# Kernel optimization log

Hardware: AMD Instinct MI355X
Metric: run time of the kernel (lower is better)

The kernel has to match this reference:

```python
import jax, jax.numpy as jnp
import numpy as np
from math import factorial, sqrt

BATCH = 4096
RS_IN = [(16, 0), (16, 1), (16, 2)]   # (mul, l), parity 0
RS_OUT = [(16, 0), (16, 1), (16, 2)]

# selection rule: l_filter in [|l_in-l_out|, l_in+l_out]
SET_LF = sorted({l for (_, li) in RS_IN for (_, lo) in RS_OUT
                 for l in range(abs(li - lo), li + lo + 1)})
Y_OFF = {l: sum(2 * k + 1 for k in SET_LF if k < l) for l in SET_LF}
Y_DIM = sum(2 * l + 1 for l in SET_LF)  # 25


def wigner_3j(j1, j2, j3, m1, m2, m3):
    if m1 + m2 + m3 != 0 or not (abs(j1 - j2) <= j3 <= j1 + j2):
        return 0.0
    if abs(m1) > j1 or abs(m2) > j2 or abs(m3) > j3:
        return 0.0
    f = factorial
    pre = sqrt(f(j1 + j2 - j3) * f(j1 - j2 + j3) * f(-j1 + j2 + j3) / f(j1 + j2 + j3 + 1))
    pre *= sqrt(f(j1 + m1) * f(j1 - m1) * f(j2 + m2) * f(j2 - m2) * f(j3 + m3) * f(j3 - m3))
    s = 0.0
    for t in range(max(0, j2 - j3 - m1, j1 - j3 + m2),
                   min(j1 + j2 - j3, j1 - m1, j2 + m2) + 1):
        s += (-1) ** t / (f(t) * f(j3 - j2 + m1 + t) * f(j3 - j1 - m2 + t)
                          * f(j1 + j2 - j3 - t) * f(j1 - m1 - t) * f(j2 + m2 - t))
    return (-1) ** (j1 - j2 - m3) * pre * s


def real_to_complex(l):
    # A[M+l, m+l]: complex Y^M expressed in the real SH basis
    A = np.zeros((2 * l + 1, 2 * l + 1), dtype=np.complex128)
    A[l, l] = 1.0
    s2 = 1.0 / np.sqrt(2.0)
    for m in range(1, l + 1):
        A[l + m, l + m] = (-1) ** m * s2
        A[l + m, l - m] = 1j * (-1) ** m * s2
        A[l - m, l + m] = s2
        A[l - m, l - m] = -1j * s2
    return A


def clebsch_gordan(l1, l2, l3):
    # real, unit-Frobenius-norm invariant 3-tensor (unique up to sign)
    T = np.zeros((2 * l1 + 1, 2 * l2 + 1, 2 * l3 + 1))
    for m1 in range(-l1, l1 + 1):
        for m2 in range(-l2, l2 + 1):
            m3 = -(m1 + m2)
            if abs(m3) <= l3:
                T[m1 + l1, m2 + l2, m3 + l3] = wigner_3j(l1, l2, l3, m1, m2, m3)
    A1, A2, A3 = real_to_complex(l1), real_to_complex(l2), real_to_complex(l3)
    C = np.einsum('abc,ai,bj,ck->ijk', T, A1.conj(), A2.conj(), A3.conj())
    C = C.real if np.linalg.norm(C.real) >= np.linalg.norm(C.imag) else C.imag
    n = np.linalg.norm(C)
    return (C / n).astype(np.float32) if n > 0 else C.astype(np.float32)


# precompute per-block padded CG tensors and R offsets
R_OFF = {}
C_BLOCKS = {}
_off = 0
for _i, (_mo, _lo) in enumerate(RS_OUT):
    for _j, (_mi, _li) in enumerate(RS_IN):
        _lfs = list(range(abs(_li - _lo), _li + _lo + 1))
        R_OFF[(_i, _j)] = (_off, len(_lfs))
        _off += _mo * _mi * len(_lfs)
        _C = np.zeros((len(_lfs), 2 * _lo + 1, 2 * _li + 1, Y_DIM), dtype=np.float32)
        for _k, _lf in enumerate(_lfs):
            _o = Y_OFF[_lf]
            _C[_k, :, :, _o:_o + 2 * _lf + 1] = clebsch_gordan(_lo, _li, _lf)
        C_BLOCKS[(_i, _j)] = jnp.asarray(_C)
N_PATH = _off  # 4864


def setup_inputs() -> dict:
    key = jax.random.key(0)
    k1, k2, k3 = jax.random.split(key, 3)
    Y = jax.random.normal(k1, (Y_DIM, BATCH), dtype=jnp.float32)
    R = jax.random.normal(k2, (BATCH, N_PATH), dtype=jnp.float32)
    norm_coef = jax.random.uniform(k3, (len(RS_OUT), len(RS_IN), BATCH),
                                   dtype=jnp.float32, minval=0.5, maxval=1.5)
    return {"Y": Y, "R": R, "norm_coef": norm_coef}


def reference(Y, R, norm_coef):
    # Y: [Y_DIM, batch], R: [batch, N_PATH], norm_coef: [3, 3, batch]
    batch = Y.shape[1]
    rows = []
    for i, (mo, lo) in enumerate(RS_OUT):
        row = []
        for j, (mi, li) in enumerate(RS_IN):
            off, nlf = R_OFF[(i, j)]
            sub_R = R[:, off:off + mo * mi * nlf].reshape(batch, mo, mi, nlf)
            # fuse the per-l_filter loop into one contraction over k and m
            K = jnp.einsum('kijm,mz,zuvk,z->zuivj',
                           C_BLOCKS[(i, j)], Y, sub_R, norm_coef[i, j])
            row.append(K.reshape(batch, mo * (2 * lo + 1), mi * (2 * li + 1)))
        rows.append(jnp.concatenate(row, axis=2))
    return jnp.concatenate(rows, axis=1)  # [batch, 144, 144]
```

## Files before the change

kernel.cpp:

```cpp
#include <hip/hip_runtime.h>

#define NPATH 4864
#define YDIM  25
#define NW    259
#define NCG   1225
#define NWP   400


struct Tables {
    float cg[NCG];
    int   woff[NW];
    int   wlf[NW];
    int   wij[NW];
    int   wdst[NW];
};

constexpr double cfact(int n) { double f = 1.0; for (int i = 2; i <= n; ++i) f *= (double)i; return f; }

constexpr double csqrt_(double x) {
    if (x <= 0.0) return 0.0;
    double g = x > 1.0 ? x : 1.0, p = 0.0;
    for (int it = 0; it < 200; ++it) { p = g; g = 0.5 * (g + x / g); if (g == p) break; }
    return g;
}
constexpr int cabs_(int x) { return x < 0 ? -x : x; }
constexpr int cmax3(int a, int b, int c) { int m = a > b ? a : b; return m > c ? m : c; }
constexpr int cmin3(int a, int b, int c) { int m = a < b ? a : b; return m < c ? m : c; }

constexpr double cwig3j(int j1, int j2, int j3, int m1, int m2, int m3) {
    if (m1 + m2 + m3 != 0) return 0.0;
    if (cabs_(m1) > j1 || cabs_(m2) > j2 || cabs_(m3) > j3) return 0.0;
    if (j3 < cabs_(j1 - j2) || j3 > j1 + j2) return 0.0;
    double prod = cfact(j1 + j2 - j3) * cfact(j1 - j2 + j3) * cfact(-j1 + j2 + j3)
                / cfact(j1 + j2 + j3 + 1);
    prod *= cfact(j1 + m1) * cfact(j1 - m1) * cfact(j2 + m2) * cfact(j2 - m2)
          * cfact(j3 + m3) * cfact(j3 - m3);
    double pre = csqrt_(prod);
    int t0 = cmax3(0, j2 - j3 - m1, j1 - j3 + m2);
    int t1 = cmin3(j1 + j2 - j3, j1 - m1, j2 + m2);
    double s = 0.0;
    for (int t = t0; t <= t1; ++t) {
        double d = cfact(t) * cfact(j3 - j2 + m1 + t) * cfact(j3 - j1 - m2 + t)
                 * cfact(j1 + j2 - j3 - t) * cfact(j1 - m1 - t) * cfact(j2 + m2 - t);
        s += ((t & 1) ? -1.0 : 1.0) / d;
    }
    int p = j1 - j2 - m3; p = ((p % 2) + 2) % 2;
    return (p ? -1.0 : 1.0) * pre * s;
}

struct Ent { int col; double re; double im; };

constexpr int arow(int l, int a, Ent* e) {
    int m = a - l;
    double s2 = csqrt_(0.5);
    if (m == 0) { e[0] = Ent{l, 1.0, 0.0}; return 1; }
    if (m > 0) {
        double sgn = (m & 1) ? -1.0 : 1.0;
        e[0] = Ent{l + m, sgn * s2, 0.0};
        e[1] = Ent{l - m, 0.0, sgn * s2};
        return 2;
    }
    int mm = -m;
    e[0] = Ent{l + mm, s2, 0.0};
    e[1] = Ent{l - mm, 0.0, -s2};
    return 2;
}

constexpr Tables make_tables() {
    Tables T{};
    const int CL1[19]  = {0,0,0,1,1,1,1,1,1,1,2,2,2,2,2,2,2,2,2};
    const int CL2[19]  = {0,1,2,0,1,1,1,2,2,2,0,1,1,1,2,2,2,2,2};
    const int CL3[19]  = {0,1,2,1,0,1,2,1,2,3,2,1,2,3,0,1,2,3,4};
    const int COFF[19] = {0,1,10,35,44,53,80,125,170,245,350,375,420,495,600,625,700,825,1000};

    for (int c = 0; c < 19; ++c) {
        int l1 = CL1[c], l2 = CL2[c], l3 = CL3[c], coff = COFF[c];
        int n1 = 2 * l1 + 1, n2 = 2 * l2 + 1, n3 = 2 * l3 + 1, ntot = n1 * n2 * n3;
        double Cre[225] = {}, Cim[225] = {};
        for (int a = 0; a < n1; ++a)
            for (int b = 0; b < n2; ++b) {
                int m1 = a - l1, m2 = b - l2, m3 = -(m1 + m2);
                if (cabs_(m3) > l3) continue;
                double tv = cwig3j(l1, l2, l3, m1, m2, m3);
                if (tv == 0.0) continue;
                int crow = m3 + l3;
                Ent e1[2] = {}, e2[2] = {}, e3[2] = {};
                int k1 = arow(l1, a, e1), k2 = arow(l2, b, e2), k3 = arow(l3, crow, e3);
                for (int x = 0; x < k1; ++x)
                    for (int y = 0; y < k2; ++y)
                        for (int w = 0; w < k3; ++w) {
                            double r1 = e1[x].re, i1 = -e1[x].im;
                            double r2 = e2[y].re, i2 = -e2[y].im;
                            double r3 = e3[w].re, i3 = -e3[w].im;
                            double pr = r1 * r2 - i1 * i2, pi = r1 * i2 + i1 * r2;
                            double qr = pr * r3 - pi * i3, qi = pr * i3 + pi * r3;
                            int idx = (e1[x].col * n2 + e2[y].col) * n3 + e3[w].col;
                            Cre[idx] += tv * qr;
                            Cim[idx] += tv * qi;
                        }
            }
        double sR = 0.0, sI = 0.0;
        for (int i = 0; i < ntot; ++i) { sR += Cre[i] * Cre[i]; sI += Cim[i] * Cim[i]; }
        bool useRe = (sR >= sI);
        double nn = csqrt_(useRe ? sR : sI);
        double inv = nn > 0.0 ? 1.0 / nn : 0.0;
        for (int i = 0; i < ntot; ++i)
            T.cg[coff + i] = (float)((useRe ? Cre[i] : Cim[i]) * inv);
    }

    const int NLFt[9]   = {1,1,1,1,3,3,1,3,5};
    const int CGOFF9[9] = {0,1,10,35,44,125,350,375,600};
    const int WPB[9]  = {0, 4, 8, 16, 20, 56, 128, 136, 200};
    const int PADt[9] = {1, 4, 8,  1,  4,  8,   1,   4,   8};
    int w = 0;
    for (int ij = 0; ij < 9; ++ij) {
        int lo = ij / 3, li = ij % 3;
        int lfmin = lo > li ? lo - li : li - lo;
        int no2 = 2 * lo + 1, ni2 = 2 * li + 1, cgo = CGOFF9[ij];
        for (int k = 0; k < NLFt[ij]; ++k) {
            int lf = lfmin + k;
            for (int a = 0; a < no2; ++a)
                for (int b = 0; b < ni2; ++b) {
                    T.woff[w] = cgo + (a * ni2 + b) * (2 * lf + 1);
                    T.wlf[w]  = lf;
                    T.wij[w]  = ij;
                    T.wdst[w] = WPB[ij] + (k * no2 + a) * PADt[ij] + b;
                    ++w;
                }
            cgo += no2 * ni2 * (2 * lf + 1);
        }
    }
    return T;
}

constexpr Tables H_TAB = make_tables();
__device__ __constant__ Tables d_tab = H_TAB;

template <int I, int J, int NLF, int WPB, int PAD, int ROFF, int ROWB, int COLB>
__device__ __forceinline__ void region(const float* __restrict__ Wp,
                                       const float* __restrict__ Rl,
                                       float* __restrict__ Oz, int u, int v) {
    constexpr int NO2 = 2 * I + 1, NI2 = 2 * J + 1;
    const float* rb = Rl + ROFF + (u * 16 + v) * NLF;
    float Rk[NLF];
#pragma unroll
    for (int k = 0; k < NLF; ++k) Rk[k] = rb[k];

    float acc[NO2][NI2];
#pragma unroll
    for (int a = 0; a < NO2; ++a)
#pragma unroll
        for (int b = 0; b < NI2; ++b) acc[a][b] = 0.f;

#pragma unroll
    for (int k = 0; k < NLF; ++k)
#pragma unroll
        for (int a = 0; a < NO2; ++a) {
            const float* wrow = Wp + WPB + (k * NO2 + a) * PAD;
            if constexpr (NI2 == 1) {
                acc[a][0] += wrow[0] * Rk[k];
            } else if constexpr (NI2 == 3) {
                float4 w4 = *(const float4*)wrow;
                acc[a][0] += w4.x * Rk[k];
                acc[a][1] += w4.y * Rk[k];
                acc[a][2] += w4.z * Rk[k];
            } else {
                float4 w4 = *(const float4*)wrow;
                float  w5 = wrow[4];
                acc[a][0] += w4.x * Rk[k];
                acc[a][1] += w4.y * Rk[k];
                acc[a][2] += w4.z * Rk[k];
                acc[a][3] += w4.w * Rk[k];
                acc[a][4] += w5   * Rk[k];
            }
        }

    float* ob = Oz + (ROWB + u * NO2) * 144 + COLB + v * NI2;
#pragma unroll
    for (int a = 0; a < NO2; ++a)
#pragma unroll
        for (int b = 0; b < NI2; ++b) ob[a * 144 + b] = acc[a][b];
}


__global__ __launch_bounds__(256) void tp_kernel(const float* __restrict__ Yg,
                                                 const float* __restrict__ Rg,
                                                 const float* __restrict__ Ng,
                                                 float* __restrict__ Og, int batch) {
    __shared__ __align__(16) float Rl[NPATH];
    __shared__ __align__(16) float Wp[NWP];
    __shared__ float Ys[YDIM];
    __shared__ float Ns[9];

    int z = blockIdx.x;
    int t = threadIdx.x;

    const float4* Rg4 = (const float4*)(Rg + (size_t)z * NPATH);
    float4* Rl4 = (float4*)Rl;
    for (int p = t; p < NPATH / 4; p += 256) Rl4[p] = Rg4[p];
    if (t < YDIM) Ys[t] = Yg[t * batch + z];
    if (t >= 32 && t < 41) Ns[t - 32] = Ng[(t - 32) * batch + z];
    __syncthreads();

    for (int w = t; w < NW; w += 256) {
        int off = d_tab.woff[w], lf = d_tab.wlf[w];
        float acc = 0.f;
        for (int ci = 0; ci <= 2 * lf; ++ci) acc += d_tab.cg[off + ci] * Ys[lf * lf + ci];
        Wp[d_tab.wdst[w]] = acc * Ns[d_tab.wij[w]];
    }
    __syncthreads();

    float* Oz = Og + (size_t)z * 20736;
    int u = t >> 4, v = t & 15;

    region<0, 0, 1,   0, 1,     0,  0,  0>(Wp, Rl, Oz, u, v);
    region<0, 1, 1,   4, 4,   256,  0, 16>(Wp, Rl, Oz, u, v);
    region<0, 2, 1,   8, 8,   512,  0, 64>(Wp, Rl, Oz, u, v);
    region<1, 0, 1,  16, 1,   768, 16,  0>(Wp, Rl, Oz, u, v);
    region<1, 1, 3,  20, 4,  1024, 16, 16>(Wp, Rl, Oz, u, v);
    region<1, 2, 3,  56, 8,  1792, 16, 64>(Wp, Rl, Oz, u, v);
    region<2, 0, 1, 128, 1,  2560, 64,  0>(Wp, Rl, Oz, u, v);
    region<2, 1, 3, 136, 4,  2816, 64, 16>(Wp, Rl, Oz, u, v);
    region<2, 2, 5, 200, 8,  3584, 64, 64>(Wp, Rl, Oz, u, v);
}

extern "C" void kernel_launch(void* const* d_in, const int* in_sizes, int n_in,
                              void* d_out, int out_size, void* d_ws, size_t ws_size,
                              hipStream_t stream) {
    const float* Y = (const float*)d_in[0];
    const float* R = (const float*)d_in[1];
    const float* N = (const float*)d_in[2];
    float* O = (float*)d_out;
    int batch = in_sizes[0] / YDIM;

    hipLaunchKernelGGL(tp_kernel, dim3(batch), dim3(256), 0, stream, Y, R, N, O, batch);
}
```

Measured before the change: 417.1 us.

## Split each batch element across two 128-thread blocks and read R directly from global

```diff
diff --git a/kernel.cpp b/kernel.cpp
--- a/kernel.cpp
+++ b/kernel.cpp
@@ -138,10 +138,10 @@
 
 template <int I, int J, int NLF, int WPB, int PAD, int ROFF, int ROWB, int COLB>
 __device__ __forceinline__ void region(const float* __restrict__ Wp,
-                                       const float* __restrict__ Rl,
+                                       const float* __restrict__ Rz,
                                        float* __restrict__ Oz, int u, int v) {
     constexpr int NO2 = 2 * I + 1, NI2 = 2 * J + 1;
-    const float* rb = Rl + ROFF + (u * 16 + v) * NLF;
+    const float* rb = Rz + ROFF + (u * 16 + v) * NLF;
     float Rk[NLF];
 #pragma unroll
     for (int k = 0; k < NLF; ++k) Rk[k] = rb[k];
@@ -183,45 +183,39 @@
 }
 
 
-__global__ __launch_bounds__(256) void tp_kernel(const float* __restrict__ Yg,
+__global__ __launch_bounds__(128) void tp_kernel(const float* __restrict__ Yg,
                                                  const float* __restrict__ Rg,
                                                  const float* __restrict__ Ng,
                                                  float* __restrict__ Og, int batch) {
-    __shared__ __align__(16) float Rl[NPATH];
     __shared__ __align__(16) float Wp[NWP];
-    __shared__ float Ys[YDIM];
-    __shared__ float Ns[9];
-
-    int z = blockIdx.x;
+
+    int bid = blockIdx.x;
+    int z = bid >> 1, h = bid & 1;
     int t = threadIdx.x;
 
-    const float4* Rg4 = (const float4*)(Rg + (size_t)z * NPATH);
-    float4* Rl4 = (float4*)Rl;
-    for (int p = t; p < NPATH / 4; p += 256) Rl4[p] = Rg4[p];
-    if (t < YDIM) Ys[t] = Yg[t * batch + z];
-    if (t >= 32 && t < 41) Ns[t - 32] = Ng[(t - 32) * batch + z];
-    __syncthreads();
-
-    for (int w = t; w < NW; w += 256) {
+    for (int w = t; w < NW; w += 128) {
         int off = d_tab.woff[w], lf = d_tab.wlf[w];
         float acc = 0.f;
-        for (int ci = 0; ci <= 2 * lf; ++ci) acc += d_tab.cg[off + ci] * Ys[lf * lf + ci];
-        Wp[d_tab.wdst[w]] = acc * Ns[d_tab.wij[w]];
+        int yb = lf * lf;
+        for (int ci = 0; ci <= 2 * lf; ++ci)
+            acc += d_tab.cg[off + ci] * Yg[(yb + ci) * batch + z];
+        Wp[d_tab.wdst[w]] = acc * Ng[d_tab.wij[w] * batch + z];
     }
     __syncthreads();
 
+    const float* Rz = Rg + (size_t)z * NPATH;
     float* Oz = Og + (size_t)z * 20736;
-    int u = t >> 4, v = t & 15;
-
-    region<0, 0, 1,   0, 1,     0,  0,  0>(Wp, Rl, Oz, u, v);
-    region<0, 1, 1,   4, 4,   256,  0, 16>(Wp, Rl, Oz, u, v);
-    region<0, 2, 1,   8, 8,   512,  0, 64>(Wp, Rl, Oz, u, v);
-    region<1, 0, 1,  16, 1,   768, 16,  0>(Wp, Rl, Oz, u, v);
-    region<1, 1, 3,  20, 4,  1024, 16, 16>(Wp, Rl, Oz, u, v);
-    region<1, 2, 3,  56, 8,  1792, 16, 64>(Wp, Rl, Oz, u, v);
-    region<2, 0, 1, 128, 1,  2560, 64,  0>(Wp, Rl, Oz, u, v);
-    region<2, 1, 3, 136, 4,  2816, 64, 16>(Wp, Rl, Oz, u, v);
-    region<2, 2, 5, 200, 8,  3584, 64, 64>(Wp, Rl, Oz, u, v);
+    int u = (h << 3) | (t >> 4), v = t & 15;
+
+    region<0, 0, 1,   0, 1,     0,  0,  0>(Wp, Rz, Oz, u, v);
+    region<0, 1, 1,   4, 4,   256,  0, 16>(Wp, Rz, Oz, u, v);
+    region<0, 2, 1,   8, 8,   512,  0, 64>(Wp, Rz, Oz, u, v);
+    region<1, 0, 1,  16, 1,   768, 16,  0>(Wp, Rz, Oz, u, v);
+    region<1, 1, 3,  20, 4,  1024, 16, 16>(Wp, Rz, Oz, u, v);
+    region<1, 2, 3,  56, 8,  1792, 16, 64>(Wp, Rz, Oz, u, v);
+    region<2, 0, 1, 128, 1,  2560, 64,  0>(Wp, Rz, Oz, u, v);
+    region<2, 1, 3, 136, 4,  2816, 64, 16>(Wp, Rz, Oz, u, v);
+    region<2, 2, 5, 200, 8,  3584, 64, 64>(Wp, Rz, Oz, u, v);
 }
 
 extern "C" void kernel_launch(void* const* d_in, const int* in_sizes, int n_in,
@@ -233,5 +227,5 @@
     float* O = (float*)d_out;
     int batch = in_sizes[0] / YDIM;
 
-    hipLaunchKernelGGL(tp_kernel, dim3(batch), dim3(256), 0, stream, Y, R, N, O, batch);
-}
+    hipLaunchKernelGGL(tp_kernel, dim3(batch * 2), dim3(128), 0, stream, Y, R, N, O, batch);
+}
```

Measured after the change: 449.7 us. 7.8% more time.
